# Kernel optimization log

Hardware: AMD Instinct MI355X
Metric: run time of the kernel (lower is better)

## Reference

```python
import jax, jax.numpy as jnp
import numpy as np
import math

D_MODEL = 256
PRED_LEN = 256
K = 32
LOW_FREQ = 1


def setup_inputs() -> dict:
    key = jax.random.key(0)
    x = jax.random.normal(key, (8, 1024, D_MODEL), dtype=jnp.float32)
    return {"x": x}


def reference(x):
    """x: (b, t, d) -> reconstructed/extrapolated series (b, t+pred_len, d)."""
    b, t, d = x.shape
    k_ = K  # K < t//2, so the explicit-k branch of the torch module is taken

    x_freq = jnp.fft.rfft(x, axis=1)  # (b, t//2+1, d) complex
    if t % 2 == 0:
        x_freq_high = x_freq[:, LOW_FREQ:-1]  # drop DC..low_freq-1 and Nyquist
    else:
        x_freq_high = x_freq[:, LOW_FREQ:]

    # top-k magnitudes over the frequency axis, independently per (b, d)
    mag = jnp.abs(x_freq_high)                                   # (b, F, d)
    _, idx = jax.lax.top_k(jnp.transpose(mag, (0, 2, 1)), k_)    # (b, d, k)
    idx = jnp.transpose(idx, (0, 2, 1)) + LOW_FREQ               # (b, k, d) into x_freq

    x_freq_topk = jnp.take_along_axis(x_freq, idx, axis=1)       # (b, k, d) complex
    freqs = jnp.fft.rfftfreq(t).astype(x.dtype)                  # (t//2+1,)
    f_topk = freqs[idx]                                          # (b, k, d)

    # append conjugate / negative-frequency pair for a real reconstruction
    x_ext = jnp.concatenate([x_freq_topk, jnp.conj(x_freq_topk)], axis=1)  # (b, 2k, d)
    f_ext = jnp.concatenate([f_topk, -f_topk], axis=1)                     # (b, 2k, d)

    t_val = jnp.arange(t + PRED_LEN, dtype=x.dtype)              # (T,)
    amp = (jnp.abs(x_ext) / t)[:, :, None, :]                    # (b, 2k, 1, d)
    phase = jnp.angle(x_ext)[:, :, None, :]                      # (b, 2k, 1, d)
    arg = (2.0 * math.pi) * f_ext[:, :, None, :] * t_val[None, None, :, None] + phase
    x_time = amp * jnp.cos(arg)                                  # (b, 2k, T, d)
    return jnp.sum(x_time, axis=1)                               # (b, T, d)
```

## Files before the change

kernel.cpp:

```cpp
#include <hip/hip_runtime.h>
#include <math.h>

#define T_LEN 1024
#define PRED_LEN 256
#define OUT_T (T_LEN + PRED_LEN)
#define DM 256
#define KSEL 32

#define RTAU 1e-4f

#define SPAD(i) ((i) + ((i) >> 5))

__device__ __constant__ float W16RF[16] = {
    1.0f,  0.92387953f,  0.70710678f,  0.38268343f, 0.0f, -0.38268343f, -0.70710678f, -0.92387953f,
   -1.0f, -0.92387953f, -0.70710678f, -0.38268343f, 0.0f,  0.38268343f,  0.70710678f,  0.92387953f };
__device__ __constant__ float W16IF[16] = {
    0.0f, -0.38268343f, -0.70710678f, -0.92387953f, -1.0f, -0.92387953f, -0.70710678f, -0.38268343f,
    0.0f,  0.38268343f,  0.70710678f,  0.92387953f,  1.0f,  0.92387953f,  0.70710678f,  0.38268343f };

__global__ void fl_twiddle_kernel(double* __restrict__ gwr, double* __restrict__ gwi,
                                  float* __restrict__ gwrF, float* __restrict__ gwiF) {
    int e = blockIdx.x * 64 + threadIdx.x;
    double ang = (double)e * (6.283185307179586476925286766559 / 1024.0);
    double c = cos(ang), s = -sin(ang);
    gwr[e] = c; gwi[e] = s;
    gwrF[e] = (float)c; gwiF[e] = (float)s;
}

__device__ __forceinline__ void fft1024(const float2* __restrict__ xin,
                                        const float* __restrict__ twR,
                                        const float* __restrict__ twI,
                                        int lane, int w, float* ar, float* ai) {
    float Fr[4][4], Fi[4][4];
#pragma unroll
    for (int n1a = 0; n1a < 4; ++n1a) {
        float2 a  = xin[lane + 64 * (n1a + 0)];
        float2 bb = xin[lane + 64 * (n1a + 4)];
        float2 cV = xin[lane + 64 * (n1a + 8)];
        float2 d  = xin[lane + 64 * (n1a + 12)];
        float t0r = a.x + cV.x, t0i = a.y + cV.y;
        float t1r = a.x - cV.x, t1i = a.y - cV.y;
        float t2r = bb.x + d.x, t2i = bb.y + d.y;
        float t3r = bb.x - d.x, t3i = bb.y - d.y;
        Fr[n1a][0] = t0r + t2r;  Fi[n1a][0] = t0i + t2i;
        Fr[n1a][2] = t0r - t2r;  Fi[n1a][2] = t0i - t2i;
        Fr[n1a][1] = t1r + t3i;  Fi[n1a][1] = t1i - t3r;
        Fr[n1a][3] = t1r - t3i;  Fi[n1a][3] = t1i + t3r;
    }
#pragma unroll
    for (int q = 0; q < 4; ++q) {
        const int k1 = (w << 2) | q;
        float cr = Fr[0][q], ci = Fi[0][q];
#pragma unroll
        for (int n1a = 1; n1a < 4; ++n1a) {
            int e = (n1a * k1) & 15;
            float wr = W16RF[e], wi = W16IF[e];
            cr += Fr[n1a][q] * wr - Fi[n1a][q] * wi;
            ci += Fr[n1a][q] * wi + Fi[n1a][q] * wr;
        }
        int et = (lane * k1) & 1023;
        float twr = twR[SPAD(et)], twi = twI[SPAD(et)];
        ar[q] = cr * twr - ci * twi;
        ai[q] = cr * twi + ci * twr;
    }
#pragma unroll
    for (int s = 0; s < 6; ++s) {
        const int half = 32 >> s;
        const int e = (lane & (half - 1)) << s;
        const float wr = twR[SPAD(e << 4)];
        const float wi = twI[SPAD(e << 4)];
        const bool up = (lane & half) != 0;
#pragma unroll
        for (int q = 0; q < 4; ++q) {
            float orr = __shfl_xor(ar[q], half);
            float oii = __shfl_xor(ai[q], half);
            float sr = ar[q] + orr, si = ai[q] + oii;
            float dr = orr - ar[q], di = oii - ai[q];
            float ur = dr * wr - di * wi;
            float ui = dr * wi + di * wr;
            ar[q] = up ? ur : sr;
            ai[q] = up ? ui : si;
        }
    }
}

__global__ void __launch_bounds__(256, 4)
fl_fused_kernel(const float* __restrict__ x,
                const double* __restrict__ gwr, const double* __restrict__ gwi,
                const float* __restrict__ gwrF, const float* __restrict__ gwiF,
                float* __restrict__ out) {
    __shared__ float twR[SPAD(1023) + 1], twI[SPAD(1023) + 1];
    __shared__ float spR[SPAD(1023) + 1], spI[SPAD(1023) + 1];
    __shared__ char smemU[8192];
    __shared__ unsigned selw[64];
    float2* xsh  = (float2*)smemU;
    float*  mg   = (float*)smemU;
    int*    hist = (int*)(smemU + 4096);

    const int tid  = threadIdx.x;
    const int lane = tid & 63;
    const int w    = tid >> 6;

    const int bid = blockIdx.x;
    const int sp  = ((bid & 7) << 7) | (bid >> 3);
    const int b   = sp >> 7;
    const int d0  = (sp & 127) << 1;

    for (int j = 0; j < 4; ++j) {
        int e = tid + (j << 8);
        twR[SPAD(e)] = gwrF[e];
        twI[SPAD(e)] = gwiF[e];
        xsh[e] = *reinterpret_cast<const float2*>(&x[(((size_t)(b << 10) + e) << 8) + d0]);
    }
    if (tid < 64) selw[tid] = 0u;
    __syncthreads();

    float ar[4], ai[4];
    fft1024(xsh, twR, twI, lane, w, ar, ai);

    const int krev = (int)(__brev((unsigned)lane) >> 26);
    __syncthreads();
#pragma unroll
    for (int q = 0; q < 4; ++q) {
        int k = ((w << 2) | q) + (krev << 4);
        spR[SPAD(k)] = ar[q];
        spI[SPAD(k)] = ai[q];
    }
    __syncthreads();

#pragma unroll
    for (int h = 0; h < 2; ++h) {
        int m = tid + (h << 8);
        int n = (1024 - m) & 1023;
        float rm = spR[SPAD(m)], iv = spI[SPAD(m)];
        float rn = spR[SPAD(n)], in_ = spI[SPAD(n)];
        float rr0 = 0.5f * (rm + rn),  ii0 = 0.5f * (iv - in_);
        float rr1 = 0.5f * (iv + in_), ii1 = 0.5f * (rn - rm);
        mg[m]       = rr0 * rr0 + ii0 * ii0;
        mg[512 + m] = rr1 * rr1 + ii1 * ii1;
    }
    __syncthreads();

    if (tid < 128) {
        const int c = tid >> 6;
        const float* mgc = mg + (c << 9);
        int* histc = hist + (c << 8);

        float v[8]; int hiw[8];
#pragma unroll
        for (int q = 0; q < 8; ++q) v[q] = mgc[(q << 6) | lane];
        if (lane == 0) v[0] = -1.0f;
#pragma unroll
        for (int q = 0; q < 8; ++q) hiw[q] = __float_as_int(v[q]);

        int mx = hiw[0];
#pragma unroll
        for (int q = 1; q < 8; ++q) mx = max(mx, hiw[q]);
#pragma unroll
        for (int off = 1; off < 64; off <<= 1) mx = max(mx, __shfl_xor(mx, off));

        const int base = (mx >> 20) - 250;
        int idx[8];
#pragma unroll
        for (int q = 0; q < 8; ++q) {
            int t = (hiw[q] >> 20) - base;
            idx[q] = t < 0 ? 0 : t;
        }

        *reinterpret_cast<int4*>(&histc[lane << 2]) = int4{0, 0, 0, 0};
#pragma unroll
        for (int q = 0; q < 8; ++q) atomicAdd(&histc[idx[q]], 1);

        int4 cc = *reinterpret_cast<int4*>(&histc[lane << 2]);
        int s_local = cc.x + cc.y + cc.z + cc.w;

        int s = s_local;
#pragma unroll
        for (int off = 1; off < 64; off <<= 1) {
            int t = __shfl_down(s, off);
            if (lane + off < 64) s += t;
        }
        const int S_gt = s - s_local;
        const int A3 = S_gt;
        const int A2 = A3 + cc.w;
        const int A1 = A2 + cc.z;
        const int A0 = A1 + cc.y;

        int foundB = -1, foundR = 0;
        if (A0 < KSEL && A0 + cc.x >= KSEL) { foundB = (lane << 2) | 0; foundR = KSEL - A0; }
        if (A1 < KSEL && A1 + cc.y >= KSEL) { foundB = (lane << 2) | 1; foundR = KSEL - A1; }
        if (A2 < KSEL && A2 + cc.z >= KSEL) { foundB = (lane << 2) | 2; foundR = KSEL - A2; }
        if (A3 < KSEL && A3 + cc.w >= KSEL) { foundB = (lane << 2) | 3; foundR = KSEL - A3; }

        unsigned long long fm = __ballot(foundB >= 0);
        const int srcB = (int)(__ffsll((unsigned long long)fm) - 1);
        const int B = __shfl(foundB, srcB);
        const int r = __shfl(foundR, srcB);

        unsigned selmask = 0, candmask = 0;
#pragma unroll
        for (int q = 0; q < 8; ++q) {
            if (idx[q] > B) selmask |= (1u << q);
            else if (idx[q] == B) candmask |= (1u << q);
        }

        for (int it = 0; it < r; ++it) {
            float bv = -2.0f; int bq = -1;
#pragma unroll
            for (int q = 0; q < 8; ++q) {
                bool cand = ((candmask >> q) & 1u) != 0;
                if (cand && v[q] > bv) { bv = v[q]; bq = q; }
            }
            int bi = (bq < 0) ? 0x7FFFFFFF : ((bq << 6) | lane);
#pragma unroll
            for (int off = 1; off < 64; off <<= 1) {
                float ov = __shfl_xor(bv, off);
                int   oi = __shfl_xor(bi, off);
                if (ov > bv || (ov == bv && oi < bi)) { bv = ov; bi = oi; }
            }
            if (bi != 0x7FFFFFFF && lane == (bi & 63)) {
                unsigned bit = 1u << (bi >> 6);
                selmask  |= bit;
                candmask &= ~bit;
            }
        }

        {
            float vminS = 3.0e38f, vmaxU = -3.0e38f;
#pragma unroll
            for (int q = 0; q < 8; ++q) {
                if ((selmask >> q) & 1u) vminS = fminf(vminS, v[q]);
                else                     vmaxU = fmaxf(vmaxU, v[q]);
            }
#pragma unroll
            for (int off = 1; off < 64; off <<= 1) {
                vminS = fminf(vminS, __shfl_xor(vminS, off));
                vmaxU = fmaxf(vmaxU, __shfl_xor(vmaxU, off));
            }
            const float tau = RTAU * vminS;
            if (vminS - vmaxU < tau) {
                const float lo = vmaxU - tau, hi = vminS + tau;
                unsigned candq = 0; int nAbove = 0;
#pragma unroll
                for (int q = 0; q < 8; ++q) {
                    bool inw = (v[q] >= lo) && (v[q] <= hi);
                    if (inw) candq |= (1u << q);
                    if (((selmask >> q) & 1u) && v[q] > hi) ++nAbove;
                }
#pragma unroll
                for (int off = 1; off < 64; off <<= 1) nAbove += __shfl_xor(nAbove, off);
                const int kneed = KSEL - nAbove;
                selmask &= ~candq;

                const float* xcol = x + ((size_t)(b << 10) << 8) + d0 + c;
                double sV = -1.0; int sSrc = 0; int cnum = 0;
                for (int q = 0; q < 8; ++q) {
                    unsigned long long bal = __ballot((candq >> q) & 1u);
                    while (bal) {
                        int srcl = (int)(__ffsll(bal) - 1);
                        bal &= bal - 1;
                        int m = (q << 6) | srcl;
                        double sr = 0.0, si = 0.0;
                        for (int u = 0; u < 16; ++u) {
                            int n = lane + (u << 6);
                            double xvd = (double)xcol[(size_t)n << 8];
                            int e = (m * n) & 1023;
                            sr = fma(xvd, gwr[e], sr);
                            si = fma(xvd, gwi[e], si);
                        }
#pragma unroll
                        for (int off = 1; off < 64; off <<= 1) {
                            sr += __shfl_xor(sr, off);
                            si += __shfl_xor(si, off);
                        }
                        if (lane == cnum) { sV = sr * sr + si * si; sSrc = (q << 6) | srcl; }
                        ++cnum;
                        if (cnum >= 64) break;
                    }
                    if (cnum >= 64) break;
                }
                for (int it = 0; it < kneed; ++it) {
                    double bv = sV; int bl = lane;
#pragma unroll
                    for (int off = 1; off < 64; off <<= 1) {
                        double ov = __shfl_xor(bv, off);
                        int    ol = __shfl_xor(bl, off);
                        if (ov > bv || (ov == bv && ol < bl)) { bv = ov; bl = ol; }
                    }
                    int wsrc = __shfl(sSrc, bl);
                    if (lane == (wsrc & 63)) selmask |= 1u << (wsrc >> 6);
                    if (lane == bl) sV = -2.0;
                }
            }
        }

#pragma unroll
        for (int q = 0; q < 8; ++q) {
            if ((selmask >> q) & 1u) {
                int m  = (q << 6) | lane;
                int mm = 1024 - m;
                atomicOr(&selw[(c << 5) | (m  >> 5)], 1u << (m  & 31));
                atomicOr(&selw[(c << 5) | (mm >> 5)], 1u << (mm & 31));
            }
        }
    }
    __syncthreads();

    {
        float2* zc = (float2*)smemU;
#pragma unroll
        for (int jj = 0; jj < 4; ++jj) {
            int k = tid + (jj << 8);
            int n = (1024 - k) & 1023;
            float Pkr = spR[SPAD(k)], Pki = spI[SPAD(k)];
            float Pnr = spR[SPAD(n)], Pni = spI[SPAD(n)];
            float X0r = 0.5f * (Pkr + Pnr), X0i = 0.5f * (Pki - Pni);
            float X1r = 0.5f * (Pki + Pni), X1i = 0.5f * (Pnr - Pkr);
            bool s0 = (selw[(k >> 5)]      >> (k & 31)) & 1u;
            bool s1 = (selw[32 + (k >> 5)] >> (k & 31)) & 1u;
            float Zr = (s0 ? X0r : 0.0f) - (s1 ? X1i : 0.0f);
            float Zi = (s0 ? X0i : 0.0f) + (s1 ? X1r : 0.0f);
            zc[k] = float2{ Zr, -Zi };
        }
    }
    __syncthreads();

    fft1024(xsh, twR, twI, lane, w, ar, ai);

    {
        const float S = 1.0f / 1024.0f;
        float2* o2 = reinterpret_cast<float2*>(out + (size_t)b * OUT_T * DM + d0);
#pragma unroll
        for (int q = 0; q < 4; ++q) {
            int t = ((w << 2) | q) + (krev << 4);
            float2 o{ ar[q] * S, -ai[q] * S };
            o2[(size_t)t * 128] = o;
            if (t < PRED_LEN) o2[(size_t)(t + T_LEN) * 128] = o;
        }
    }
}

extern "C" void kernel_launch(void* const* d_in, const int* in_sizes, int n_in,
                              void* d_out, int out_size, void* d_ws, size_t ws_size,
                              hipStream_t stream) {
    const float* x = (const float*)d_in[0];
    float* out = (float*)d_out;

    char* w = (char*)d_ws;
    double* gwr  = (double*)(w);
    double* gwi  = (double*)(w + 1024 * sizeof(double));
    float*  gwrF = (float*)(w + 2048 * sizeof(double));
    float*  gwiF = (float*)(w + 2048 * sizeof(double) + 1024 * sizeof(float));

    hipLaunchKernelGGL(fl_twiddle_kernel, dim3(16), dim3(64), 0, stream, gwr, gwi, gwrF, gwiF);
    hipLaunchKernelGGL(fl_fused_kernel, dim3(1024), dim3(256), 0, stream,
                       x, gwr, gwi, gwrF, gwiF, out);
}
```

Measured before the change: 42.41 us.

## Use half-length complex FFT per column with real-FFT split instead of paired columns

Replaces the old scheme, which packed two d-columns into one complex 1024-point FFT, with a scheme that handles one column per block. Even and odd time samples are packed into a 512-point complex FFT, and a split/twiddle post-step produces the real spectrum. The inverse path mirrors this with a pre-step before a 512-point FFT. The grid doubles to 2048 blocks, each using less shared memory and launch bounds raised to 8 waves per SIMD, aiming for more occupancy and parallelism. The top-k selection now runs on a single wavefront per block. Costs are strided scalar global loads and stores per column instead of float2 pairs, plus the extra split arithmetic.

```diff
diff --git a/kernel.cpp b/kernel.cpp
--- a/kernel.cpp
+++ b/kernel.cpp
@@ -6,17 +6,14 @@
 #define OUT_T (T_LEN + PRED_LEN)
 #define DM 256
 #define KSEL 32
-
 #define RTAU 1e-4f
 
-#define SPAD(i) ((i) + ((i) >> 5))
-
-__device__ __constant__ float W16RF[16] = {
-    1.0f,  0.92387953f,  0.70710678f,  0.38268343f, 0.0f, -0.38268343f, -0.70710678f, -0.92387953f,
-   -1.0f, -0.92387953f, -0.70710678f, -0.38268343f, 0.0f,  0.38268343f,  0.70710678f,  0.92387953f };
-__device__ __constant__ float W16IF[16] = {
-    0.0f, -0.38268343f, -0.70710678f, -0.92387953f, -1.0f, -0.92387953f, -0.70710678f, -0.38268343f,
-    0.0f,  0.38268343f,  0.70710678f,  0.92387953f,  1.0f,  0.92387953f,  0.70710678f,  0.38268343f };
+#define SPAD(i)  ((i) + ((i) >> 5))
+#define PAD16(i) ((i) + ((i) >> 4))
+
+#define R2F 0.70710678118654752440f
+__device__ __constant__ float W8RF[8] = { 1.f,  R2F, 0.f, -R2F, -1.f, -R2F, 0.f,  R2F };
+__device__ __constant__ float W8IF[8] = { 0.f, -R2F, -1.f, -R2F, 0.f,  R2F, 1.f,  R2F };
 
 __global__ void fl_twiddle_kernel(double* __restrict__ gwr, double* __restrict__ gwi,
                                   float* __restrict__ gwrF, float* __restrict__ gwiF) {
@@ -27,38 +24,26 @@
     gwrF[e] = (float)c; gwiF[e] = (float)s;
 }
 
-__device__ __forceinline__ void fft1024(const float2* __restrict__ xin,
-                                        const float* __restrict__ twR,
-                                        const float* __restrict__ twI,
-                                        int lane, int w, float* ar, float* ai) {
-    float Fr[4][4], Fi[4][4];
-#pragma unroll
-    for (int n1a = 0; n1a < 4; ++n1a) {
-        float2 a  = xin[lane + 64 * (n1a + 0)];
-        float2 bb = xin[lane + 64 * (n1a + 4)];
-        float2 cV = xin[lane + 64 * (n1a + 8)];
-        float2 d  = xin[lane + 64 * (n1a + 12)];
-        float t0r = a.x + cV.x, t0i = a.y + cV.y;
-        float t1r = a.x - cV.x, t1i = a.y - cV.y;
-        float t2r = bb.x + d.x, t2i = bb.y + d.y;
-        float t3r = bb.x - d.x, t3i = bb.y - d.y;
-        Fr[n1a][0] = t0r + t2r;  Fi[n1a][0] = t0i + t2i;
-        Fr[n1a][2] = t0r - t2r;  Fi[n1a][2] = t0i - t2i;
-        Fr[n1a][1] = t1r + t3i;  Fi[n1a][1] = t1i - t3r;
-        Fr[n1a][3] = t1r - t3i;  Fi[n1a][3] = t1i + t3r;
-    }
-#pragma unroll
-    for (int q = 0; q < 4; ++q) {
-        const int k1 = (w << 2) | q;
-        float cr = Fr[0][q], ci = Fi[0][q];
-#pragma unroll
-        for (int n1a = 1; n1a < 4; ++n1a) {
-            int e = (n1a * k1) & 15;
-            float wr = W16RF[e], wi = W16IF[e];
-            cr += Fr[n1a][q] * wr - Fi[n1a][q] * wi;
-            ci += Fr[n1a][q] * wi + Fi[n1a][q] * wr;
-        }
-        int et = (lane * k1) & 1023;
+__device__ __forceinline__ void fft512(const float2* __restrict__ zin,
+                                       const float* __restrict__ twR,
+                                       const float* __restrict__ twI,
+                                       int lane, int w, float2* out2) {
+    float2 zv[8];
+#pragma unroll
+    for (int n1 = 0; n1 < 8; ++n1) zv[n1] = zin[PAD16(lane + (n1 << 6))];
+    float ar[2], ai[2];
+#pragma unroll
+    for (int q = 0; q < 2; ++q) {
+        const int k1 = (w << 1) | q;
+        float cr = 0.f, ci = 0.f;
+#pragma unroll
+        for (int n1 = 0; n1 < 8; ++n1) {
+            int e = (k1 * n1) & 7;
+            float wr = W8RF[e], wi = W8IF[e];
+            cr += zv[n1].x * wr - zv[n1].y * wi;
+            ci += zv[n1].x * wi + zv[n1].y * wr;
+        }
+        int et = (lane * k1) << 1;
         float twr = twR[SPAD(et)], twi = twI[SPAD(et)];
         ar[q] = cr * twr - ci * twi;
         ai[q] = cr * twi + ci * twr;
@@ -71,84 +56,89 @@
         const float wi = twI[SPAD(e << 4)];
         const bool up = (lane & half) != 0;
 #pragma unroll
-        for (int q = 0; q < 4; ++q) {
+        for (int q = 0; q < 2; ++q) {
             float orr = __shfl_xor(ar[q], half);
             float oii = __shfl_xor(ai[q], half);
             float sr = ar[q] + orr, si = ai[q] + oii;
             float dr = orr - ar[q], di = oii - ai[q];
-            float ur = dr * wr - di * wi;
-            float ui = dr * wi + di * wr;
-            ar[q] = up ? ur : sr;
-            ai[q] = up ? ui : si;
-        }
-    }
+            ar[q] = up ? (dr * wr - di * wi) : sr;
+            ai[q] = up ? (dr * wi + di * wr) : si;
+        }
+    }
+    out2[0] = float2{ ar[0], ai[0] };
+    out2[1] = float2{ ar[1], ai[1] };
 }
 
-__global__ void __launch_bounds__(256, 4)
+__global__ void __launch_bounds__(256, 8)
 fl_fused_kernel(const float* __restrict__ x,
                 const double* __restrict__ gwr, const double* __restrict__ gwi,
                 const float* __restrict__ gwrF, const float* __restrict__ gwiF,
                 float* __restrict__ out) {
     __shared__ float twR[SPAD(1023) + 1], twI[SPAD(1023) + 1];
-    __shared__ float spR[SPAD(1023) + 1], spI[SPAD(1023) + 1];
-    __shared__ char smemU[8192];
-    __shared__ unsigned selw[64];
-    float2* xsh  = (float2*)smemU;
-    float*  mg   = (float*)smemU;
-    int*    hist = (int*)(smemU + 4096);
+    __shared__ float2 regA[PAD16(511) + 1];
+    __shared__ float2 spX[PAD16(511) + 1];
+    __shared__ unsigned selw[16];
 
     const int tid  = threadIdx.x;
     const int lane = tid & 63;
     const int w    = tid >> 6;
 
     const int bid = blockIdx.x;
-    const int sp  = ((bid & 7) << 7) | (bid >> 3);
-    const int b   = sp >> 7;
-    const int d0  = (sp & 127) << 1;
+    const int sp  = ((bid & 7) << 8) | (bid >> 3);
+    const int b   = sp >> 8;
+    const int d   = sp & 255;
 
     for (int j = 0; j < 4; ++j) {
         int e = tid + (j << 8);
         twR[SPAD(e)] = gwrF[e];
         twI[SPAD(e)] = gwiF[e];
-        xsh[e] = *reinterpret_cast<const float2*>(&x[(((size_t)(b << 10) + e) << 8) + d0]);
-    }
-    if (tid < 64) selw[tid] = 0u;
-    __syncthreads();
-
-    float ar[4], ai[4];
-    fft1024(xsh, twR, twI, lane, w, ar, ai);
-
+    }
+    {
+        const float* xc = x + (((size_t)b << 10) << 8) + d;
+        for (int j = 0; j < 2; ++j) {
+            int n = tid + (j << 8);
+            float xe = xc[(size_t)(2 * n) << 8];
+            float xo = xc[(size_t)(2 * n + 1) << 8];
+            regA[PAD16(n)] = float2{ xe, xo };
+        }
+    }
+    if (tid < 16) selw[tid] = 0u;
+    __syncthreads();
+
+    float2 zo[2];
+    fft512(regA, twR, twI, lane, w, zo);
     const int krev = (int)(__brev((unsigned)lane) >> 26);
     __syncthreads();
 #pragma unroll
-    for (int q = 0; q < 4; ++q) {
-        int k = ((w << 2) | q) + (krev << 4);
-        spR[SPAD(k)] = ar[q];
-        spI[SPAD(k)] = ai[q];
-    }
-    __syncthreads();
-
-#pragma unroll
-    for (int h = 0; h < 2; ++h) {
-        int m = tid + (h << 8);
-        int n = (1024 - m) & 1023;
-        float rm = spR[SPAD(m)], iv = spI[SPAD(m)];
-        float rn = spR[SPAD(n)], in_ = spI[SPAD(n)];
-        float rr0 = 0.5f * (rm + rn),  ii0 = 0.5f * (iv - in_);
-        float rr1 = 0.5f * (iv + in_), ii1 = 0.5f * (rn - rm);
-        mg[m]       = rr0 * rr0 + ii0 * ii0;
-        mg[512 + m] = rr1 * rr1 + ii1 * ii1;
-    }
-    __syncthreads();
-
-    if (tid < 128) {
-        const int c = tid >> 6;
-        const float* mgc = mg + (c << 9);
-        int* histc = hist + (c << 8);
+    for (int q = 0; q < 2; ++q) {
+        int k = ((w << 1) | q) + (krev << 3);
+        regA[PAD16(k)] = zo[q];
+    }
+    __syncthreads();
+
+    for (int j = 0; j < 2; ++j) {
+        int k = tid + (j << 8);
+        int kk = (512 - k) & 511;
+        float2 Zk = regA[PAD16(k)];
+        float2 Zm = regA[PAD16(kk)];
+        float Er = 0.5f * (Zk.x + Zm.x), Ei = 0.5f * (Zk.y - Zm.y);
+        float Dr = 0.5f * (Zk.x - Zm.x), Di = 0.5f * (Zk.y + Zm.y);
+        float Or = Di, Oi = -Dr;
+        float wr = twR[SPAD(k)], wi = twI[SPAD(k)];
+        spX[PAD16(k)] = float2{ Er + (Or * wr - Oi * wi),
+                                Ei + (Or * wi + Oi * wr) };
+    }
+    __syncthreads();
+
+    if (tid < 64) {
+        int* histc = (int*)&regA[0];
 
         float v[8]; int hiw[8];
 #pragma unroll
-        for (int q = 0; q < 8; ++q) v[q] = mgc[(q << 6) | lane];
+        for (int q = 0; q < 8; ++q) {
+            float2 X = spX[PAD16((q << 6) | lane)];
+            v[q] = X.x * X.x + X.y * X.y;
+        }
         if (lane == 0) v[0] = -1.0f;
 #pragma unroll
         for (int q = 0; q < 8; ++q) hiw[q] = __float_as_int(v[q]);
@@ -252,7 +242,7 @@
                 const int kneed = KSEL - nAbove;
                 selmask &= ~candq;
 
-                const float* xcol = x + ((size_t)(b << 10) << 8) + d0 + c;
+                const float* xcol = x + (((size_t)b << 10) << 8) + d;
                 double sV = -1.0; int sSrc = 0; int cnum = 0;
                 for (int q = 0; q < 8; ++q) {
                     unsigned long long bal = __ballot((candq >> q) & 1u);
@@ -297,45 +287,49 @@
 #pragma unroll
         for (int q = 0; q < 8; ++q) {
             if ((selmask >> q) & 1u) {
-                int m  = (q << 6) | lane;
-                int mm = 1024 - m;
-                atomicOr(&selw[(c << 5) | (m  >> 5)], 1u << (m  & 31));
-                atomicOr(&selw[(c << 5) | (mm >> 5)], 1u << (mm & 31));
-            }
-        }
-    }
-    __syncthreads();
-
+                int m = (q << 6) | lane;
+                atomicOr(&selw[m >> 5], 1u << (m & 31));
+            }
+        }
+    }
+    __syncthreads();
+
+    for (int j = 0; j < 2; ++j) {
+        int k = tid + (j << 8);
+        float2 g{ 0.f, 0.f };
+        if (k != 0) {
+            int kk = 512 - k;
+            bool sk  = (selw[k  >> 5] >> (k  & 31)) & 1u;
+            bool skk = (selw[kk >> 5] >> (kk & 31)) & 1u;
+            float2 Yk = spX[PAD16(k)];  if (!sk)  Yk = float2{ 0.f, 0.f };
+            float2 Ym = spX[PAD16(kk)]; if (!skk) Ym = float2{ 0.f, 0.f };
+            float Epr = 0.5f * (Yk.x + Ym.x), Epi = 0.5f * (Yk.y - Ym.y);
+            float Dpr = 0.5f * (Yk.x - Ym.x), Dpi = 0.5f * (Yk.y + Ym.y);
+            float wr = twR[SPAD(k)], wi = -twI[SPAD(k)];
+            float Opr = Dpr * wr - Dpi * wi;
+            float Opi = Dpr * wi + Dpi * wr;
+            g = float2{ Epr - Opi, -(Epi + Opr) };
+        }
+        regA[PAD16(k)] = g;
+    }
+    __syncthreads();
+
+    float2 co[2];
+    fft512(regA, twR, twI, lane, w, co);
     {
-        float2* zc = (float2*)smemU;
-#pragma unroll
-        for (int jj = 0; jj < 4; ++jj) {
-            int k = tid + (jj << 8);
-            int n = (1024 - k) & 1023;
-            float Pkr = spR[SPAD(k)], Pki = spI[SPAD(k)];
-            float Pnr = spR[SPAD(n)], Pni = spI[SPAD(n)];
-            float X0r = 0.5f * (Pkr + Pnr), X0i = 0.5f * (Pki - Pni);
-            float X1r = 0.5f * (Pki + Pni), X1i = 0.5f * (Pnr - Pkr);
-            bool s0 = (selw[(k >> 5)]      >> (k & 31)) & 1u;
-            bool s1 = (selw[32 + (k >> 5)] >> (k & 31)) & 1u;
-            float Zr = (s0 ? X0r : 0.0f) - (s1 ? X1i : 0.0f);
-            float Zi = (s0 ? X0i : 0.0f) + (s1 ? X1r : 0.0f);
-            zc[k] = float2{ Zr, -Zi };
-        }
-    }
-    __syncthreads();
-
-    fft1024(xsh, twR, twI, lane, w, ar, ai);
-
-    {
-        const float S = 1.0f / 1024.0f;
-        float2* o2 = reinterpret_cast<float2*>(out + (size_t)b * OUT_T * DM + d0);
-#pragma unroll
-        for (int q = 0; q < 4; ++q) {
-            int t = ((w << 2) | q) + (krev << 4);
-            float2 o{ ar[q] * S, -ai[q] * S };
-            o2[(size_t)t * 128] = o;
-            if (t < PRED_LEN) o2[(size_t)(t + T_LEN) * 128] = o;
+        const float S = 1.0f / 512.0f;
+        float* ob = out + ((size_t)b * OUT_T) * DM + d;
+#pragma unroll
+        for (int q = 0; q < 2; ++q) {
+            int n = ((w << 1) | q) + (krev << 3);
+            float y0 = co[q].x * S;
+            float y1 = -co[q].y * S;
+            ob[(size_t)(2 * n)     << 8] = y0;
+            ob[(size_t)(2 * n + 1) << 8] = y1;
+            if (n < 128) {
+                ob[(size_t)(2 * n + T_LEN)     << 8] = y0;
+                ob[(size_t)(2 * n + 1 + T_LEN) << 8] = y1;
+            }
         }
     }
 }
@@ -353,6 +347,6 @@
     float*  gwiF = (float*)(w + 2048 * sizeof(double) + 1024 * sizeof(float));
 
     hipLaunchKernelGGL(fl_twiddle_kernel, dim3(16), dim3(64), 0, stream, gwr, gwi, gwrF, gwiF);
-    hipLaunchKernelGGL(fl_fused_kernel, dim3(1024), dim3(256), 0, stream,
+    hipLaunchKernelGGL(fl_fused_kernel, dim3(2048), dim3(256), 0, stream,
                        x, gwr, gwi, gwrF, gwiF, out);
 }
```

New measurement: 70.09 us. +65.3%, slower.
